# Performance work log

Measured on AMD Instinct MI355X. Metric: run time of the kernel, lower is better.

Reference implementation:

```python
import jax, jax.numpy as jnp
import numpy as np

N_NODES = 100000
N_EDGES = 1600000
IN_FEATS = 128
N_HIDDEN = 128
N_CLASSES = 16


def setup_inputs() -> dict:
    key = jax.random.key(0)
    ks = jax.random.split(key, 10)
    features = jax.random.normal(ks[0], (N_NODES, IN_FEATS), dtype=jnp.float32)
    src = jax.random.randint(ks[1], (N_EDGES,), 0, N_NODES, dtype=jnp.int32)
    dst = jax.random.randint(ks[2], (N_EDGES,), 0, N_NODES, dtype=jnp.int32)
    # Glorot-ish init for the three GraphConv layers
    def glorot(k, fan_in, fan_out):
        s = (2.0 / (fan_in + fan_out)) ** 0.5
        return jax.random.normal(k, (fan_in, fan_out), dtype=jnp.float32) * s
    W0 = glorot(ks[3], IN_FEATS, N_HIDDEN)
    b0 = jnp.zeros((N_HIDDEN,), jnp.float32)
    W1 = glorot(ks[4], N_HIDDEN, N_HIDDEN)
    b1 = jnp.zeros((N_HIDDEN,), jnp.float32)
    W2 = glorot(ks[5], N_HIDDEN, N_CLASSES)
    b2 = jnp.zeros((N_CLASSES,), jnp.float32)
    return {"features": features, "src": src, "dst": dst,
            "W0": W0, "b0": b0, "W1": W1, "b1": b1, "W2": W2, "b2": b2}


def _graph_conv(h, src, dst, src_norm, dst_norm, W, b, act):
    # DGL GraphConv, norm='both':
    # out = D_dst^{-1/2} * sum_{(u->v) in E} (D_src^{-1/2} h)_u W  + b
    h = h * src_norm[:, None]           # [N, F] scale by out-degree^-1/2
    hw = h @ W                          # [N, F_out] transform before gather (F_out <= F here)
    agg = jax.ops.segment_sum(hw[src], dst, num_segments=h.shape[0])  # scatter-add over edges
    out = agg * dst_norm[:, None] + b
    return act(out)


def reference(features, src, dst, W0, b0, W1, b1, W2, b2):
    N = features.shape[0]
    ones = jnp.ones(src.shape[0], dtype=jnp.float32)
    out_deg = jnp.clip(jax.ops.segment_sum(ones, src, num_segments=N), 1.0)
    in_deg = jnp.clip(jax.ops.segment_sum(ones, dst, num_segments=N), 1.0)
    src_norm = out_deg ** -0.5
    dst_norm = in_deg ** -0.5

    relu = jax.nn.relu
    pos_sigmoid = lambda x: jax.nn.sigmoid(x) + 1e-8

    h = features.astype(jnp.float32)
    h = _graph_conv(h, src, dst, src_norm, dst_norm, W0, b0, relu)
    h = _graph_conv(h, src, dst, src_norm, dst_norm, W1, b1, relu)
    h = _graph_conv(h, src, dst, src_norm, dst_norm, W2, b2, pos_sigmoid)
    return h
```

## Files before the change

kernel.cpp:

```cpp
#include <hip/hip_runtime.h>
#include <hip/hip_bf16.h>


constexpr int BLK = 256;
constexpr int CH = 8192;

typedef __attribute__((ext_vector_type(8))) short s8v;
typedef __attribute__((ext_vector_type(4))) float f4v;

__device__ __forceinline__ float bflo(unsigned int u) { return __uint_as_float(u << 16); }
__device__ __forceinline__ float bfhi(unsigned int u) { return __uint_as_float(u & 0xffff0000u); }
__device__ __forceinline__ unsigned int bfr(float f) {
    unsigned int u = __float_as_uint(f);
    return (u + 0x7fffu + ((u >> 16) & 1u)) >> 16;
}
__device__ __forceinline__ unsigned int bfpack(float lo, float hi) {
    unsigned int ul = __float_as_uint(lo), uh = __float_as_uint(hi);
    unsigned int rl = (ul + 0x7fffu + ((ul >> 16) & 1u)) >> 16;
    unsigned int rh = (uh + 0x7fffu + ((uh >> 16) & 1u)) & 0xffff0000u;
    return rl | rh;
}

__global__ __launch_bounds__(256) void k_pcount(const int* __restrict__ src, const int* __restrict__ dst,
                                                int* __restrict__ pmat_d, int* __restrict__ pmat_s,
                                                int E, int NB) {
    __shared__ int hd[1024], hs[1024];
    for (int i = threadIdx.x; i < 1024; i += 256) { hd[i] = 0; hs[i] = 0; }
    __syncthreads();
    int b = blockIdx.x;
    int e0 = b * CH, e1 = min(e0 + CH, E);
    for (int e = e0 + threadIdx.x; e < e1; e += 256) {
        atomicAdd(&hd[dst[e] >> 7], 1);
        atomicAdd(&hs[src[e] >> 7], 1);
    }
    __syncthreads();
    for (int i = threadIdx.x; i < NB; i += 256) {
        pmat_d[(size_t)b * NB + i] = hd[i];
        pmat_s[(size_t)b * NB + i] = hs[i];
    }
}

__global__ __launch_bounds__(1024) void k_pscan1(const int* __restrict__ pmat_d, const int* __restrict__ pmat_s,
                                                 int* __restrict__ bbase_d, int* __restrict__ bbase_s,
                                                 int NB, int nblk) {
    const int* pmat = blockIdx.x ? pmat_s : pmat_d;
    int* bbase = blockIdx.x ? bbase_s : bbase_d;
    __shared__ int s[1024];
    int t = threadIdx.x;
    int tot = 0;
    if (t < NB) {
#pragma unroll 8
        for (int b = 0; b < nblk; b++) tot += pmat[(size_t)b * NB + t];
    }
    s[t] = (t < NB) ? tot : 0;
    __syncthreads();
    for (int d = 1; d < 1024; d <<= 1) {
        int x = (t >= d) ? s[t - d] : 0;
        __syncthreads();
        s[t] += x;
        __syncthreads();
    }
    if (t < NB) {
        bbase[t] = s[t] - tot;
        if (t == NB - 1) bbase[NB] = s[t];
    }
}

__global__ __launch_bounds__(256) void k_pscan2(const int* __restrict__ pmat_d, const int* __restrict__ pmat_s,
                                                const int* __restrict__ bbase_d, const int* __restrict__ bbase_s,
                                                int* __restrict__ omat_d, int* __restrict__ omat_s,
                                                int NB, int nblk) {
    int which = blockIdx.x & 1;
    int t = (blockIdx.x >> 1) * 256 + threadIdx.x;
    const int* pmat = which ? pmat_s : pmat_d;
    const int* bbase = which ? bbase_s : bbase_d;
    int* omat = which ? omat_s : omat_d;
    if (t >= NB) return;
    int run = bbase[t];
#pragma unroll 8
    for (int b = 0; b < nblk; b++) {
        size_t idx = (size_t)b * NB + t;
        omat[idx] = run;
        run += pmat[idx];
    }
}

__global__ __launch_bounds__(256) void k_pscatter(const int* __restrict__ src, const int* __restrict__ dst,
                                                  const int* __restrict__ omat_d, const int* __restrict__ omat_s,
                                                  unsigned int* __restrict__ ebuf_d, unsigned char* __restrict__ ebuf_s,
                                                  int E, int NB) {
    __shared__ int cd[1024], cs[1024];
    int b = blockIdx.x;
    for (int i = threadIdx.x; i < NB; i += 256) {
        cd[i] = omat_d[(size_t)b * NB + i];
        cs[i] = omat_s[(size_t)b * NB + i];
    }
    __syncthreads();
    int e0 = b * CH, e1 = min(e0 + CH, E);
    for (int e = e0 + threadIdx.x; e < e1; e += 256) {
        int s_ = src[e], d_ = dst[e];
        int pd = atomicAdd(&cd[d_ >> 7], 1);
        ebuf_d[pd] = (unsigned)s_ | ((unsigned)(d_ & 127) << 17);
        int ps = atomicAdd(&cs[s_ >> 7], 1);
        ebuf_s[ps] = (unsigned char)(s_ & 127);
    }
}

__global__ __launch_bounds__(256) void k_bcount(const unsigned char* __restrict__ ebuf_s,
                                                const int* __restrict__ bbase_s,
                                                float* __restrict__ srcn, int N) {
    __shared__ int cnt[128];
    int k = blockIdx.x;
    if (threadIdx.x < 128) cnt[threadIdx.x] = 0;
    __syncthreads();
    int beg = bbase_s[k], end = bbase_s[k + 1];
    for (int i = beg + threadIdx.x; i < end; i += 256) atomicAdd(&cnt[ebuf_s[i]], 1);
    __syncthreads();
    if (threadIdx.x < 128) {
        int v = k * 128 + threadIdx.x;
        if (v < N) {
            int c = cnt[threadIdx.x];
            if (c < 1) c = 1;
            srcn[v] = rsqrtf((float)c);
        }
    }
}

__global__ void k_wt3(const float* __restrict__ W0, const float* __restrict__ W1, const float* __restrict__ W2,
                      unsigned short* __restrict__ Wt0, unsigned short* __restrict__ Wt1,
                      unsigned short* __restrict__ Wt2) {
    int b = blockIdx.x;
    const float* W; unsigned short* Wt; int total, base;
    if (b < 64)      { W = W0; Wt = Wt0; total = 16384; base = b * 256; }
    else if (b < 128){ W = W1; Wt = Wt1; total = 16384; base = (b - 64) * 256; }
    else             { W = W2; Wt = Wt2; total = 2048;  base = (b - 128) * 256; }
    int i = base + threadIdx.x;
    if (i < total) {
        int Ncol = total >> 7;
        int c = i >> 7, k = i & 127;
        Wt[i] = (unsigned short)bfr(W[k * Ncol + c]);
    }
}

__global__ void k_prep(const float* __restrict__ F, const float* __restrict__ srcn,
                       unsigned short* __restrict__ A0, int N) {
    int i = blockIdx.x * blockDim.x + threadIdx.x;
    if (i >= N * 16) return;
    int row = i >> 4;
    float s = srcn[row];
    const float4* p = (const float4*)(F + (size_t)i * 8);
    float4 a = p[0], b = p[1];
    uint4 o;
    o.x = bfpack(a.x * s, a.y * s);
    o.y = bfpack(a.z * s, a.w * s);
    o.z = bfpack(b.x * s, b.y * s);
    o.w = bfpack(b.z * s, b.w * s);
    *(uint4*)(A0 + (size_t)i * 8) = o;
}

template <int NT, int EPI>
__global__ __launch_bounds__(256) void k_gemm_mfma(const unsigned short* __restrict__ A,
                                                   const unsigned short* __restrict__ Wt,
                                                   const float* __restrict__ bias,
                                                   unsigned short* __restrict__ outb,
                                                   float* __restrict__ outf, int M) {
    __shared__ unsigned short As[64 * 128];
    __shared__ unsigned short Ws[NT * 16 * 128];
    int tx = threadIdx.x;
    int row0 = blockIdx.x * 64;
    for (int p = 0; p < NT; ++p) {
        int r = p * 16 + (tx >> 4);
        int c = tx & 15;
        int cs = c ^ (r & 7);
        *(uint4*)(&Ws[(r * 16 + cs) * 8]) = *(const uint4*)(Wt + (size_t)r * 128 + c * 8);
    }
    for (int p = 0; p < 4; ++p) {
        int r = p * 16 + (tx >> 4);
        int c = tx & 15;
        int cs = c ^ (r & 7);
        int gr = row0 + r;
        uint4 v = make_uint4(0u, 0u, 0u, 0u);
        if (gr < M) v = *(const uint4*)(A + (size_t)gr * 128 + c * 8);
        *(uint4*)(&As[(r * 16 + cs) * 8]) = v;
    }
    __syncthreads();

    int w = tx >> 6, l = tx & 63;
    int lr = l & 15, lg = l >> 4;
    f4v acc[NT];
#pragma unroll
    for (int nt = 0; nt < NT; ++nt) { acc[nt][0] = 0.f; acc[nt][1] = 0.f; acc[nt][2] = 0.f; acc[nt][3] = 0.f; }

    int ar = w * 16 + lr;
#pragma unroll
    for (int kk = 0; kk < 4; ++kk) {
        s8v af = *(const s8v*)(&As[(ar * 16 + ((kk * 4 + lg) ^ (ar & 7))) * 8]);
#pragma unroll
        for (int nt = 0; nt < NT; ++nt) {
            int br = nt * 16 + lr;
            s8v bf = *(const s8v*)(&Ws[(br * 16 + ((kk * 4 + lg) ^ (br & 7))) * 8]);
            acc[nt] = __builtin_amdgcn_mfma_f32_16x16x32_bf16(af, bf, acc[nt], 0, 0, 0);
        }
    }
#pragma unroll
    for (int nt = 0; nt < NT; ++nt) {
#pragma unroll
        for (int i = 0; i < 4; ++i) {
            int R = row0 + w * 16 + lg * 4 + i;
            if (R < M) {
                int col = nt * 16 + lr;
                float v = acc[nt][i];
                if (EPI == 0) {
                    outb[(size_t)R * 128 + col] = (unsigned short)bfr(v);
                } else {
                    v += bias[col];
                    v = 1.f / (1.f + __expf(-v)) + 1e-8f;
                    outf[(size_t)R * 16 + col] = v;
                }
            }
        }
    }
}

template <int EPI>
__global__ __launch_bounds__(256) void k_bagg(const unsigned short* __restrict__ hw,
                                              const unsigned int* __restrict__ ebuf,
                                              const int* __restrict__ bbase,
                                              const float* __restrict__ srcn,
                                              const float* __restrict__ bias,
                                              unsigned short* __restrict__ out, int N) {
    __shared__ unsigned int rec[4096];
    __shared__ unsigned int sorted[4096];
    __shared__ int cnt[128];
    __shared__ int wstart[129];
    __shared__ int wcur[128];
    int k = blockIdx.x;
    int tx = threadIdx.x;
    int ebeg = bbase[k];
    int ecnt = bbase[k + 1] - ebeg;
    if (ecnt > 4096) ecnt = 4096;
    if (tx < 128) cnt[tx] = 0;
    __syncthreads();
    for (int i = tx; i < ecnt; i += 256) {
        unsigned int r = ebuf[ebeg + i];
        rec[i] = r;
        atomicAdd(&cnt[(r >> 17) & 127], 1);
    }
    __syncthreads();
    if (tx < 128) wcur[tx] = cnt[tx];
    __syncthreads();
    for (int d = 1; d < 128; d <<= 1) {
        int x = (tx < 128 && tx >= d) ? wcur[tx - d] : 0;
        __syncthreads();
        if (tx < 128) wcur[tx] += x;
        __syncthreads();
    }
    if (tx < 128) wstart[tx] = wcur[tx] - cnt[tx];
    if (tx == 127) wstart[128] = wcur[127];
    __syncthreads();
    if (tx < 128) wcur[tx] = wstart[tx];
    __syncthreads();
    for (int i = tx; i < ecnt; i += 256) {
        unsigned int r = rec[i];
        int dl = (r >> 17) & 127;
        int p = atomicAdd(&wcur[dl], 1);
        sorted[p] = r & 0x1FFFFu;
    }
    __syncthreads();

    int g = tx >> 4, sub = tx & 15;
#pragma unroll
    for (int rep = 0; rep < 8; rep++) {
        int j = g + rep * 16;
        int v = k * 128 + j;
        if (v >= N) continue;
        int s0 = wstart[j], s1 = wstart[j + 1];
        int deg = s1 - s0;

        float a0 = 0.f, a1 = 0.f, a2 = 0.f, a3 = 0.f, a4 = 0.f, a5 = 0.f, a6 = 0.f, a7 = 0.f;
#define ACC8(V)                                                         \
        a0 += bflo(V.x); a1 += bfhi(V.x); a2 += bflo(V.y); a3 += bfhi(V.y); \
        a4 += bflo(V.z); a5 += bfhi(V.z); a6 += bflo(V.w); a7 += bfhi(V.w);
        int e = s0;
        for (; e + 4 <= s1; e += 4) {
            int x0 = sorted[e], x1 = sorted[e + 1], x2 = sorted[e + 2], x3 = sorted[e + 3];
            uint4 v0 = *(const uint4*)(hw + (size_t)x0 * 128 + sub * 8);
            uint4 v1 = *(const uint4*)(hw + (size_t)x1 * 128 + sub * 8);
            uint4 v2 = *(const uint4*)(hw + (size_t)x2 * 128 + sub * 8);
            uint4 v3 = *(const uint4*)(hw + (size_t)x3 * 128 + sub * 8);
            ACC8(v0) ACC8(v1) ACC8(v2) ACC8(v3)
        }
        for (; e < s1; ++e) {
            int x0 = sorted[e];
            uint4 v0 = *(const uint4*)(hw + (size_t)x0 * 128 + sub * 8);
            ACC8(v0)
        }
#undef ACC8
        int d = deg < 1 ? 1 : deg;
        float dn = rsqrtf((float)d);
        float o0 = a0 * dn, o1 = a1 * dn, o2 = a2 * dn, o3 = a3 * dn;
        float o4 = a4 * dn, o5 = a5 * dn, o6 = a6 * dn, o7 = a7 * dn;
        if (EPI == 0) {
            float4 b0 = *(const float4*)(bias + sub * 8);
            float4 b1 = *(const float4*)(bias + sub * 8 + 4);
            float sn = srcn[v];
            o0 = fmaxf(o0 + b0.x, 0.f) * sn; o1 = fmaxf(o1 + b0.y, 0.f) * sn;
            o2 = fmaxf(o2 + b0.z, 0.f) * sn; o3 = fmaxf(o3 + b0.w, 0.f) * sn;
            o4 = fmaxf(o4 + b1.x, 0.f) * sn; o5 = fmaxf(o5 + b1.y, 0.f) * sn;
            o6 = fmaxf(o6 + b1.z, 0.f) * sn; o7 = fmaxf(o7 + b1.w, 0.f) * sn;
        }
        uint4 o;
        o.x = bfpack(o0, o1); o.y = bfpack(o2, o3);
        o.z = bfpack(o4, o5); o.w = bfpack(o6, o7);
        *(uint4*)(out + (size_t)v * 128 + sub * 8) = o;
    }
}

extern "C" void kernel_launch(void* const* d_in, const int* in_sizes, int n_in,
                              void* d_out, int out_size, void* d_ws, size_t ws_size,
                              hipStream_t stream) {
    const float* features = (const float*)d_in[0];
    const int*   src      = (const int*)d_in[1];
    const int*   dst      = (const int*)d_in[2];
    const float* W0       = (const float*)d_in[3];
    const float* b0       = (const float*)d_in[4];
    const float* W1       = (const float*)d_in[5];
    const float* b1       = (const float*)d_in[6];
    const float* W2       = (const float*)d_in[7];
    const float* b2       = (const float*)d_in[8];
    float* out = (float*)d_out;

    const int N = in_sizes[0] / 128;
    const int E = in_sizes[1];
    const int NB = (N + 127) >> 7;
    const int nblk = (E + CH - 1) / CH;

    char* ws = (char*)d_ws;
    size_t off = 0;
    auto alloc = [&](size_t bytes) -> char* {
        char* p = ws + off;
        off += (bytes + 255) / 256 * 256;
        return p;
    };
    int* pmat_d  = (int*)alloc((size_t)nblk * NB * 4);
    int* pmat_s  = (int*)alloc((size_t)nblk * NB * 4);
    int* omat_d  = (int*)alloc((size_t)nblk * NB * 4);
    int* omat_s  = (int*)alloc((size_t)nblk * NB * 4);
    int* bbase_d = (int*)alloc((size_t)(NB + 1) * 4);
    int* bbase_s = (int*)alloc((size_t)(NB + 1) * 4);
    unsigned int*  ebuf_d = (unsigned int*)alloc((size_t)E * 4);
    unsigned char* ebuf_s = (unsigned char*)alloc((size_t)E);
    float* srcn  = (float*)alloc((size_t)N * 4);
    unsigned short* Wt0 = (unsigned short*)alloc(128 * 128 * 2);
    unsigned short* Wt1 = (unsigned short*)alloc(128 * 128 * 2);
    unsigned short* Wt2 = (unsigned short*)alloc(16 * 128 * 2);
    unsigned short* B1 = (unsigned short*)alloc((size_t)N * 128 * 2);
    unsigned short* B2 = (unsigned short*)alloc((size_t)N * 128 * 2);
    unsigned short* B3 = (unsigned short*)alloc((size_t)N * 128 * 2);
    (void)ws_size; (void)n_in; (void)out_size;

    k_pcount<<<nblk, 256, 0, stream>>>(src, dst, pmat_d, pmat_s, E, NB);
    k_pscan1<<<2, 1024, 0, stream>>>(pmat_d, pmat_s, bbase_d, bbase_s, NB, nblk);
    k_pscan2<<<2 * ((NB + 255) / 256), 256, 0, stream>>>(pmat_d, pmat_s, bbase_d, bbase_s, omat_d, omat_s, NB, nblk);
    k_pscatter<<<nblk, 256, 0, stream>>>(src, dst, omat_d, omat_s, ebuf_d, ebuf_s, E, NB);
    k_bcount<<<NB, 256, 0, stream>>>(ebuf_s, bbase_s, srcn, N);

    k_wt3<<<136, 256, 0, stream>>>(W0, W1, W2, Wt0, Wt1, Wt2);
    k_prep<<<(N * 16 + BLK - 1) / BLK, BLK, 0, stream>>>(features, srcn, B1, N);

    int gb = (N + 63) / 64;

    k_gemm_mfma<8, 0><<<gb, 256, 0, stream>>>(B1, Wt0, nullptr, B2, nullptr, N);
    k_bagg<0><<<NB, 256, 0, stream>>>(B2, ebuf_d, bbase_d, srcn, b0, B3, N);
    k_gemm_mfma<8, 0><<<gb, 256, 0, stream>>>(B3, Wt1, nullptr, B2, nullptr, N);
    k_bagg<0><<<NB, 256, 0, stream>>>(B2, ebuf_d, bbase_d, srcn, b1, B1, N);
    k_bagg<1><<<NB, 256, 0, stream>>>(B1, ebuf_d, bbase_d, nullptr, nullptr, B3, N);
    k_gemm_mfma<1, 1><<<gb, 256, 0, stream>>>(B3, Wt2, b2, nullptr, out, N);
}
```

Before: 406.4 us.

## Build CSR once, transform before aggregating in last layer, fuse feature prep into GEMM

Sorts edges into a global CSR once, instead of re-sorting each destination bucket inside every aggregation kernel. The last layer now applies the 128->16 GEMM before aggregation, so its gather moves 16-wide rows instead of 128-wide. The fp32-to-bf16 scaling of the input features is folded into the first GEMM's tile load, removing a separate pass. In exchange, the aggregation kernels run one node per 16 or 4 lanes with flat indexing and read CSR indices from global memory instead of LDS, and a new sort kernel with an extra E-sized buffer is added.

```diff
diff --git a/kernel.cpp b/kernel.cpp
--- a/kernel.cpp
+++ b/kernel.cpp
@@ -126,6 +126,54 @@
     }
 }
 
+__global__ __launch_bounds__(256) void k_sortcsr(const unsigned int* __restrict__ ebuf,
+                                                 const int* __restrict__ bbase,
+                                                 int* __restrict__ csr, int* __restrict__ rowptr,
+                                                 int N, int E) {
+    __shared__ unsigned int rec[4096];
+    __shared__ unsigned int sorted[4096];
+    __shared__ int cnt[128];
+    __shared__ int wstart[129];
+    __shared__ int wcur[128];
+    int k = blockIdx.x, tx = threadIdx.x;
+    int ebeg = bbase[k];
+    int ecnt = bbase[k + 1] - ebeg;
+    if (ecnt > 4096) ecnt = 4096;
+    if (tx < 128) cnt[tx] = 0;
+    __syncthreads();
+    for (int i = tx; i < ecnt; i += 256) {
+        unsigned int r = ebuf[ebeg + i];
+        rec[i] = r;
+        atomicAdd(&cnt[(r >> 17) & 127], 1);
+    }
+    __syncthreads();
+    if (tx < 128) wcur[tx] = cnt[tx];
+    __syncthreads();
+    for (int d = 1; d < 128; d <<= 1) {
+        int x = (tx < 128 && tx >= d) ? wcur[tx - d] : 0;
+        __syncthreads();
+        if (tx < 128) wcur[tx] += x;
+        __syncthreads();
+    }
+    if (tx < 128) wstart[tx] = wcur[tx] - cnt[tx];
+    if (tx == 127) wstart[128] = wcur[127];
+    __syncthreads();
+    if (tx < 128) wcur[tx] = wstart[tx];
+    __syncthreads();
+    for (int i = tx; i < ecnt; i += 256) {
+        unsigned int r = rec[i];
+        int p = atomicAdd(&wcur[(r >> 17) & 127], 1);
+        sorted[p] = r & 0x1FFFFu;
+    }
+    __syncthreads();
+    for (int i = tx; i < ecnt; i += 256) csr[ebeg + i] = (int)sorted[i];
+    if (tx < 128) {
+        int v = k * 128 + tx;
+        if (v < N) rowptr[v] = ebeg + wstart[tx];
+    }
+    if (k == (int)gridDim.x - 1 && tx == 0) rowptr[N] = E;
+}
+
 __global__ void k_wt3(const float* __restrict__ W0, const float* __restrict__ W1, const float* __restrict__ W2,
                       unsigned short* __restrict__ Wt0, unsigned short* __restrict__ Wt1,
                       unsigned short* __restrict__ Wt2) {
@@ -142,28 +190,12 @@
     }
 }
 
-__global__ void k_prep(const float* __restrict__ F, const float* __restrict__ srcn,
-                       unsigned short* __restrict__ A0, int N) {
-    int i = blockIdx.x * blockDim.x + threadIdx.x;
-    if (i >= N * 16) return;
-    int row = i >> 4;
-    float s = srcn[row];
-    const float4* p = (const float4*)(F + (size_t)i * 8);
-    float4 a = p[0], b = p[1];
-    uint4 o;
-    o.x = bfpack(a.x * s, a.y * s);
-    o.y = bfpack(a.z * s, a.w * s);
-    o.z = bfpack(b.x * s, b.y * s);
-    o.w = bfpack(b.z * s, b.w * s);
-    *(uint4*)(A0 + (size_t)i * 8) = o;
-}
-
-template <int NT, int EPI>
-__global__ __launch_bounds__(256) void k_gemm_mfma(const unsigned short* __restrict__ A,
+template <int NT, int F32IN>
+__global__ __launch_bounds__(256) void k_gemm_mfma(const unsigned short* __restrict__ Ab,
+                                                   const float* __restrict__ Af,
+                                                   const float* __restrict__ srcn,
                                                    const unsigned short* __restrict__ Wt,
-                                                   const float* __restrict__ bias,
-                                                   unsigned short* __restrict__ outb,
-                                                   float* __restrict__ outf, int M) {
+                                                   unsigned short* __restrict__ outb, int M) {
     __shared__ unsigned short As[64 * 128];
     __shared__ unsigned short Ws[NT * 16 * 128];
     int tx = threadIdx.x;
@@ -180,7 +212,19 @@
         int cs = c ^ (r & 7);
         int gr = row0 + r;
         uint4 v = make_uint4(0u, 0u, 0u, 0u);
-        if (gr < M) v = *(const uint4*)(A + (size_t)gr * 128 + c * 8);
+        if (gr < M) {
+            if (F32IN) {
+                const float4* pf = (const float4*)(Af + (size_t)gr * 128 + c * 8);
+                float4 a = pf[0], b = pf[1];
+                float s = srcn[gr];
+                v.x = bfpack(a.x * s, a.y * s);
+                v.y = bfpack(a.z * s, a.w * s);
+                v.z = bfpack(b.x * s, b.y * s);
+                v.w = bfpack(b.z * s, b.w * s);
+            } else {
+                v = *(const uint4*)(Ab + (size_t)gr * 128 + c * 8);
+            }
+        }
         *(uint4*)(&As[(r * 16 + cs) * 8]) = v;
     }
     __syncthreads();
@@ -209,111 +253,94 @@
             int R = row0 + w * 16 + lg * 4 + i;
             if (R < M) {
                 int col = nt * 16 + lr;
-                float v = acc[nt][i];
-                if (EPI == 0) {
-                    outb[(size_t)R * 128 + col] = (unsigned short)bfr(v);
-                } else {
-                    v += bias[col];
-                    v = 1.f / (1.f + __expf(-v)) + 1e-8f;
-                    outf[(size_t)R * 16 + col] = v;
-                }
+                outb[(size_t)R * (NT * 16) + col] = (unsigned short)bfr(acc[nt][i]);
             }
         }
     }
 }
 
-template <int EPI>
-__global__ __launch_bounds__(256) void k_bagg(const unsigned short* __restrict__ hw,
-                                              const unsigned int* __restrict__ ebuf,
-                                              const int* __restrict__ bbase,
+__global__ __launch_bounds__(256) void k_aggN(const unsigned short* __restrict__ hw,
+                                              const int* __restrict__ csr,
+                                              const int* __restrict__ rowptr,
                                               const float* __restrict__ srcn,
                                               const float* __restrict__ bias,
                                               unsigned short* __restrict__ out, int N) {
-    __shared__ unsigned int rec[4096];
-    __shared__ unsigned int sorted[4096];
-    __shared__ int cnt[128];
-    __shared__ int wstart[129];
-    __shared__ int wcur[128];
-    int k = blockIdx.x;
-    int tx = threadIdx.x;
-    int ebeg = bbase[k];
-    int ecnt = bbase[k + 1] - ebeg;
-    if (ecnt > 4096) ecnt = 4096;
-    if (tx < 128) cnt[tx] = 0;
-    __syncthreads();
-    for (int i = tx; i < ecnt; i += 256) {
-        unsigned int r = ebuf[ebeg + i];
-        rec[i] = r;
-        atomicAdd(&cnt[(r >> 17) & 127], 1);
-    }
-    __syncthreads();
-    if (tx < 128) wcur[tx] = cnt[tx];
-    __syncthreads();
-    for (int d = 1; d < 128; d <<= 1) {
-        int x = (tx < 128 && tx >= d) ? wcur[tx - d] : 0;
-        __syncthreads();
-        if (tx < 128) wcur[tx] += x;
-        __syncthreads();
-    }
-    if (tx < 128) wstart[tx] = wcur[tx] - cnt[tx];
-    if (tx == 127) wstart[128] = wcur[127];
-    __syncthreads();
-    if (tx < 128) wcur[tx] = wstart[tx];
-    __syncthreads();
-    for (int i = tx; i < ecnt; i += 256) {
-        unsigned int r = rec[i];
-        int dl = (r >> 17) & 127;
-        int p = atomicAdd(&wcur[dl], 1);
-        sorted[p] = r & 0x1FFFFu;
-    }
-    __syncthreads();
-
-    int g = tx >> 4, sub = tx & 15;
-#pragma unroll
-    for (int rep = 0; rep < 8; rep++) {
-        int j = g + rep * 16;
-        int v = k * 128 + j;
-        if (v >= N) continue;
-        int s0 = wstart[j], s1 = wstart[j + 1];
-        int deg = s1 - s0;
-
-        float a0 = 0.f, a1 = 0.f, a2 = 0.f, a3 = 0.f, a4 = 0.f, a5 = 0.f, a6 = 0.f, a7 = 0.f;
+    int t = blockIdx.x * 256 + threadIdx.x;
+    int v = t >> 4, sub = t & 15;
+    if (v >= N) return;
+    int s0 = rowptr[v], s1 = rowptr[v + 1];
+
+    float a0 = 0.f, a1 = 0.f, a2 = 0.f, a3 = 0.f, a4 = 0.f, a5 = 0.f, a6 = 0.f, a7 = 0.f;
 #define ACC8(V)                                                         \
-        a0 += bflo(V.x); a1 += bfhi(V.x); a2 += bflo(V.y); a3 += bfhi(V.y); \
-        a4 += bflo(V.z); a5 += bfhi(V.z); a6 += bflo(V.w); a7 += bfhi(V.w);
-        int e = s0;
-        for (; e + 4 <= s1; e += 4) {
-            int x0 = sorted[e], x1 = sorted[e + 1], x2 = sorted[e + 2], x3 = sorted[e + 3];
-            uint4 v0 = *(const uint4*)(hw + (size_t)x0 * 128 + sub * 8);
-            uint4 v1 = *(const uint4*)(hw + (size_t)x1 * 128 + sub * 8);
-            uint4 v2 = *(const uint4*)(hw + (size_t)x2 * 128 + sub * 8);
-            uint4 v3 = *(const uint4*)(hw + (size_t)x3 * 128 + sub * 8);
-            ACC8(v0) ACC8(v1) ACC8(v2) ACC8(v3)
-        }
-        for (; e < s1; ++e) {
-            int x0 = sorted[e];
-            uint4 v0 = *(const uint4*)(hw + (size_t)x0 * 128 + sub * 8);
-            ACC8(v0)
-        }
+    a0 += bflo(V.x); a1 += bfhi(V.x); a2 += bflo(V.y); a3 += bfhi(V.y); \
+    a4 += bflo(V.z); a5 += bfhi(V.z); a6 += bflo(V.w); a7 += bfhi(V.w);
+    int e = s0;
+    for (; e + 4 <= s1; e += 4) {
+        int x0 = csr[e], x1 = csr[e + 1], x2 = csr[e + 2], x3 = csr[e + 3];
+        uint4 v0 = *(const uint4*)(hw + (size_t)x0 * 128 + sub * 8);
+        uint4 v1 = *(const uint4*)(hw + (size_t)x1 * 128 + sub * 8);
+        uint4 v2 = *(const uint4*)(hw + (size_t)x2 * 128 + sub * 8);
+        uint4 v3 = *(const uint4*)(hw + (size_t)x3 * 128 + sub * 8);
+        ACC8(v0) ACC8(v1) ACC8(v2) ACC8(v3)
+    }
+    for (; e < s1; ++e) {
+        int x0 = csr[e];
+        uint4 v0 = *(const uint4*)(hw + (size_t)x0 * 128 + sub * 8);
+        ACC8(v0)
+    }
 #undef ACC8
-        int d = deg < 1 ? 1 : deg;
-        float dn = rsqrtf((float)d);
-        float o0 = a0 * dn, o1 = a1 * dn, o2 = a2 * dn, o3 = a3 * dn;
-        float o4 = a4 * dn, o5 = a5 * dn, o6 = a6 * dn, o7 = a7 * dn;
-        if (EPI == 0) {
-            float4 b0 = *(const float4*)(bias + sub * 8);
-            float4 b1 = *(const float4*)(bias + sub * 8 + 4);
-            float sn = srcn[v];
-            o0 = fmaxf(o0 + b0.x, 0.f) * sn; o1 = fmaxf(o1 + b0.y, 0.f) * sn;
-            o2 = fmaxf(o2 + b0.z, 0.f) * sn; o3 = fmaxf(o3 + b0.w, 0.f) * sn;
-            o4 = fmaxf(o4 + b1.x, 0.f) * sn; o5 = fmaxf(o5 + b1.y, 0.f) * sn;
-            o6 = fmaxf(o6 + b1.z, 0.f) * sn; o7 = fmaxf(o7 + b1.w, 0.f) * sn;
-        }
-        uint4 o;
-        o.x = bfpack(o0, o1); o.y = bfpack(o2, o3);
-        o.z = bfpack(o4, o5); o.w = bfpack(o6, o7);
-        *(uint4*)(out + (size_t)v * 128 + sub * 8) = o;
-    }
+    int deg = s1 - s0;
+    if (deg < 1) deg = 1;
+    float dn = rsqrtf((float)deg);
+    float4 b0 = *(const float4*)(bias + sub * 8);
+    float4 b1 = *(const float4*)(bias + sub * 8 + 4);
+    float sn = srcn[v];
+    float o0 = fmaxf(a0 * dn + b0.x, 0.f) * sn, o1 = fmaxf(a1 * dn + b0.y, 0.f) * sn;
+    float o2 = fmaxf(a2 * dn + b0.z, 0.f) * sn, o3 = fmaxf(a3 * dn + b0.w, 0.f) * sn;
+    float o4 = fmaxf(a4 * dn + b1.x, 0.f) * sn, o5 = fmaxf(a5 * dn + b1.y, 0.f) * sn;
+    float o6 = fmaxf(a6 * dn + b1.z, 0.f) * sn, o7 = fmaxf(a7 * dn + b1.w, 0.f) * sn;
+    uint4 o;
+    o.x = bfpack(o0, o1); o.y = bfpack(o2, o3);
+    o.z = bfpack(o4, o5); o.w = bfpack(o6, o7);
+    *(uint4*)(out + (size_t)v * 128 + sub * 8) = o;
+}
+
+__global__ __launch_bounds__(256) void k_agg16(const unsigned short* __restrict__ hw,
+                                               const int* __restrict__ csr,
+                                               const int* __restrict__ rowptr,
+                                               const float* __restrict__ bias,
+                                               float* __restrict__ out, int N) {
+    int t = blockIdx.x * 256 + threadIdx.x;
+    int v = t >> 2, q = t & 3;
+    if (v >= N) return;
+    int s0 = rowptr[v], s1 = rowptr[v + 1];
+    float a0 = 0.f, a1 = 0.f, a2 = 0.f, a3 = 0.f;
+#define ACC4(V)                                                         \
+    a0 += bflo(V.x); a1 += bfhi(V.x); a2 += bflo(V.y); a3 += bfhi(V.y);
+    int e = s0;
+    for (; e + 4 <= s1; e += 4) {
+        int x0 = csr[e], x1 = csr[e + 1], x2 = csr[e + 2], x3 = csr[e + 3];
+        uint2 v0 = *(const uint2*)(hw + (size_t)x0 * 16 + q * 4);
+        uint2 v1 = *(const uint2*)(hw + (size_t)x1 * 16 + q * 4);
+        uint2 v2 = *(const uint2*)(hw + (size_t)x2 * 16 + q * 4);
+        uint2 v3 = *(const uint2*)(hw + (size_t)x3 * 16 + q * 4);
+        ACC4(v0) ACC4(v1) ACC4(v2) ACC4(v3)
+    }
+    for (; e < s1; ++e) {
+        int x0 = csr[e];
+        uint2 v0 = *(const uint2*)(hw + (size_t)x0 * 16 + q * 4);
+        ACC4(v0)
+    }
+#undef ACC4
+    int deg = s1 - s0;
+    if (deg < 1) deg = 1;
+    float dn = rsqrtf((float)deg);
+    float4 b = *(const float4*)(bias + q * 4);
+    float o0 = 1.f / (1.f + __expf(-(a0 * dn + b.x))) + 1e-8f;
+    float o1 = 1.f / (1.f + __expf(-(a1 * dn + b.y))) + 1e-8f;
+    float o2 = 1.f / (1.f + __expf(-(a2 * dn + b.z))) + 1e-8f;
+    float o3 = 1.f / (1.f + __expf(-(a3 * dn + b.w))) + 1e-8f;
+    *(float4*)(out + (size_t)v * 16 + q * 4) = make_float4(o0, o1, o2, o3);
 }
 
 extern "C" void kernel_launch(void* const* d_in, const int* in_sizes, int n_in,
@@ -350,13 +377,15 @@
     int* bbase_s = (int*)alloc((size_t)(NB + 1) * 4);
     unsigned int*  ebuf_d = (unsigned int*)alloc((size_t)E * 4);
     unsigned char* ebuf_s = (unsigned char*)alloc((size_t)E);
+    int* csr     = (int*)alloc((size_t)E * 4);
+    int* rowptr  = (int*)alloc((size_t)(N + 1) * 4);
     float* srcn  = (float*)alloc((size_t)N * 4);
     unsigned short* Wt0 = (unsigned short*)alloc(128 * 128 * 2);
     unsigned short* Wt1 = (unsigned short*)alloc(128 * 128 * 2);
     unsigned short* Wt2 = (unsigned short*)alloc(16 * 128 * 2);
     unsigned short* B1 = (unsigned short*)alloc((size_t)N * 128 * 2);
     unsigned short* B2 = (unsigned short*)alloc((size_t)N * 128 * 2);
-    unsigned short* B3 = (unsigned short*)alloc((size_t)N * 128 * 2);
+    unsigned short* HW16 = (unsigned short*)alloc((size_t)N * 16 * 2);
     (void)ws_size; (void)n_in; (void)out_size;
 
     k_pcount<<<nblk, 256, 0, stream>>>(src, dst, pmat_d, pmat_s, E, NB);
@@ -364,16 +393,17 @@
     k_pscan2<<<2 * ((NB + 255) / 256), 256, 0, stream>>>(pmat_d, pmat_s, bbase_d, bbase_s, omat_d, omat_s, NB, nblk);
     k_pscatter<<<nblk, 256, 0, stream>>>(src, dst, omat_d, omat_s, ebuf_d, ebuf_s, E, NB);
     k_bcount<<<NB, 256, 0, stream>>>(ebuf_s, bbase_s, srcn, N);
-
+    k_sortcsr<<<NB, 256, 0, stream>>>(ebuf_d, bbase_d, csr, rowptr, N, E);
     k_wt3<<<136, 256, 0, stream>>>(W0, W1, W2, Wt0, Wt1, Wt2);
-    k_prep<<<(N * 16 + BLK - 1) / BLK, BLK, 0, stream>>>(features, srcn, B1, N);
 
     int gb = (N + 63) / 64;
-
-    k_gemm_mfma<8, 0><<<gb, 256, 0, stream>>>(B1, Wt0, nullptr, B2, nullptr, N);
-    k_bagg<0><<<NB, 256, 0, stream>>>(B2, ebuf_d, bbase_d, srcn, b0, B3, N);
-    k_gemm_mfma<8, 0><<<gb, 256, 0, stream>>>(B3, Wt1, nullptr, B2, nullptr, N);
-    k_bagg<0><<<NB, 256, 0, stream>>>(B2, ebuf_d, bbase_d, srcn, b1, B1, N);
-    k_bagg<1><<<NB, 256, 0, stream>>>(B1, ebuf_d, bbase_d, nullptr, nullptr, B3, N);
-    k_gemm_mfma<1, 1><<<gb, 256, 0, stream>>>(B3, Wt2, b2, nullptr, out, N);
-}
+    int anb = (N * 16 + 255) / 256;
+    int a16b = (N * 4 + 255) / 256;
+
+    k_gemm_mfma<8, 1><<<gb, 256, 0, stream>>>(nullptr, features, srcn, Wt0, B2, N);
+    k_aggN<<<anb, 256, 0, stream>>>(B2, csr, rowptr, srcn, b0, B1, N);
+    k_gemm_mfma<8, 0><<<gb, 256, 0, stream>>>(B1, nullptr, nullptr, Wt1, B2, N);
+    k_aggN<<<anb, 256, 0, stream>>>(B2, csr, rowptr, srcn, b1, B1, N);
+    k_gemm_mfma<1, 0><<<gb, 256, 0, stream>>>(B1, nullptr, nullptr, Wt2, HW16, N);
+    k_agg16<<<a16b, 256, 0, stream>>>(HW16, csr, rowptr, b2, out, N);
+}
```

Measured after the change: 351.7 us. 13.5% less time.
